# Kernel optimization log

Measured on AMD Instinct MI355X. Metric: run time of the kernel, lower is better.

## Reference

```python
import jax, jax.numpy as jnp
import numpy as np

DIM = 768        # channel dim C
HEADS = 12       # num_heads
MAXLEN = 128     # max_seq_len == window length N
NW = 64          # num_windows
B = 4            # batch


def setup_inputs() -> dict:
    key = jax.random.key(0)
    k0, k1, k2, k3 = jax.random.split(key, 4)
    B_ = NW * B
    x = jax.random.normal(k0, (B_, MAXLEN, DIM), jnp.float32)
    mask = jnp.zeros((NW, MAXLEN, MAXLEN), jnp.float32)  # 0/-inf additive window mask
    qkv_w = jax.random.normal(k1, (3 * DIM, DIM), jnp.float32) * 0.02
    bias_table = jax.random.normal(k2, (2 * MAXLEN - 1, HEADS), jnp.float32) * 0.02
    proj_w = jax.random.normal(k3, (DIM, DIM), jnp.float32) * 0.02
    proj_b = jnp.zeros((DIM,), jnp.float32)
    return {"x": x, "mask": mask, "qkv_w": qkv_w, "bias_table": bias_table,
            "proj_w": proj_w, "proj_b": proj_b}


def reference(x, mask, qkv_w, bias_table, proj_w, proj_b):
    B_, N, C = x.shape
    H = HEADS
    hd = C // H
    scale = hd ** -0.5
    # qkv projection (no bias): (B_, N, 3, H, hd)
    qkv = (x @ qkv_w.T).reshape(B_, N, 3, H, hd)
    q = qkv[:, :, 0].transpose(0, 2, 1, 3) * scale  # (B_, H, N, hd)
    k = qkv[:, :, 1].transpose(0, 2, 1, 3)
    v = qkv[:, :, 2].transpose(0, 2, 1, 3)
    attn = jnp.einsum('bhnd,bhmd->bhnm', q, k)       # (B_, H, N, N)
    # relative position bias gather
    coords = jnp.arange(N)
    rel_idx = coords[:, None] - coords[None, :] + (MAXLEN - 1)  # (N, N)
    bias = bias_table[rel_idx]                        # (N, N, H)
    attn = attn + bias.transpose(2, 0, 1)[None]       # (B_, H, N, N)
    # window mask add (mask ndim == 3 branch)
    nW = mask.shape[0]
    attn = attn.reshape(B_ // nW, nW, H, N, N) + mask[None, :, None]
    attn = jax.nn.softmax(attn.reshape(B_, H, N, N), axis=-1)
    out = jnp.einsum('bhnm,bhmd->bhnd', attn, v)      # (B_, H, N, hd)
    out = out.transpose(0, 2, 1, 3).reshape(B_, N, C)
    return out @ proj_w.T + proj_b
```

## Files before the change

### kernel.cpp

```cpp
#include <hip/hip_runtime.h>
#include <hip/hip_bf16.h>
#include <stdint.h>

typedef unsigned short u16;
typedef __bf16 bf16x8 __attribute__((ext_vector_type(8)));
typedef float f32x4 __attribute__((ext_vector_type(4)));

__device__ __forceinline__ u16 f2bf(float f) {
  union { float f; uint32_t u; } v; v.f = f;
  uint32_t u = v.u;
  return (u16)((u + 0x7FFFu + ((u >> 16) & 1u)) >> 16);
}

__device__ __forceinline__ f32x4 mfma16(bf16x8 a, bf16x8 b, f32x4 c) {
  return __builtin_amdgcn_mfma_f32_16x16x32_bf16(a, b, c, 0, 0, 0);
}

#define GLOBAL_TO_LDS16(g, l)                                                  \
  __builtin_amdgcn_global_load_lds(                                            \
      (const __attribute__((address_space(1))) void*)(g),                      \
      (__attribute__((address_space(3))) void*)(l), 16, 0, 0)

__global__ void cvt_bf16(const float* __restrict__ src, u16* __restrict__ dst, int n4) {
  int i = blockIdx.x * 256 + threadIdx.x;
  if (i < n4) {
    float4 f = ((const float4*)src)[i];
    ushort4 o;
    o.x = f2bf(f.x); o.y = f2bf(f.y); o.z = f2bf(f.z); o.w = f2bf(f.w);
    ((ushort4*)dst)[i] = o;
  }
}

__global__ __launch_bounds__(256) void qkv_gemm(
    const u16* __restrict__ A, const u16* __restrict__ Bt,
    u16* __restrict__ q, u16* __restrict__ k, u16* __restrict__ vT) {
  const int K = 768;
  __shared__ u16 As[128 * 64];
  __shared__ u16 Bs[128 * 64];
  int tid = threadIdx.x;
  int wave = tid >> 6, lane = tid & 63;
  int quad = lane >> 4, lrow = lane & 15;
  int m0 = blockIdx.y * 128, n0 = blockIdx.x * 128;
  int wr = (wave >> 1) * 64, wc = (wave & 1) * 64;

  const u16* asrc[4]; const u16* bsrc[4]; int ldst[4];
#pragma unroll
  for (int s = 0; s < 4; s++) {
    int p = (wave * 4 + s) * 64 + lane;
    int row = p >> 3, cp = p & 7;
    int c = cp ^ (row & 7);
    asrc[s] = A + (size_t)(m0 + row) * K + c * 8;
    bsrc[s] = Bt + (size_t)(n0 + row) * K + c * 8;
    ldst[s] = p * 8;
  }
  f32x4 acc[4][4] = {};
  for (int k0 = 0; k0 < K; k0 += 64) {
#pragma unroll
    for (int s = 0; s < 4; s++) {
      GLOBAL_TO_LDS16(asrc[s] + k0, As + ldst[s]);
      GLOBAL_TO_LDS16(bsrc[s] + k0, Bs + ldst[s]);
    }
    __syncthreads();
#pragma unroll
    for (int kk = 0; kk < 2; kk++) {
      bf16x8 av[4], bv[4];
#pragma unroll
      for (int i = 0; i < 4; i++) {
        int r = wr + i * 16 + lrow;
        av[i] = *(const bf16x8*)(As + r * 64 + ((((kk << 2) | quad) ^ (r & 7)) << 3));
      }
#pragma unroll
      for (int j = 0; j < 4; j++) {
        int r = wc + j * 16 + lrow;
        bv[j] = *(const bf16x8*)(Bs + r * 64 + ((((kk << 2) | quad) ^ (r & 7)) << 3));
      }
#pragma unroll
      for (int i = 0; i < 4; i++)
#pragma unroll
        for (int j = 0; j < 4; j++)
          acc[i][j] = mfma16(av[i], bv[j], acc[i][j]);
    }
    __syncthreads();
  }
#pragma unroll
  for (int j = 0; j < 4; j++) {
    int nb = n0 + wc + j * 16;
    int t = nb / 768;
    int rem = nb - t * 768;
    int h = rem >> 6;
    int d = (rem & 63) + lrow;
#pragma unroll
    for (int i = 0; i < 4; i++) {
#pragma unroll
      for (int r = 0; r < 4; r++) {
        int m = m0 + wr + i * 16 + quad * 4 + r;
        int b = m >> 7, seq = m & 127;
        size_t base = ((size_t)(b * 12 + h)) * 8192;
        float val = acc[i][j][r];
        if (t == 0)      q[base + seq * 64 + d] = f2bf(val * 0.125f);
        else if (t == 1) k[base + seq * 64 + d] = f2bf(val);
        else             vT[base + d * 128 + seq] = f2bf(val);
      }
    }
  }
}

__global__ __launch_bounds__(256) void attn_kernel(
    const u16* __restrict__ q, const u16* __restrict__ k, const u16* __restrict__ vT,
    const float* __restrict__ mask, const float* __restrict__ bias_table,
    u16* __restrict__ attn_out) {
  __shared__ u16 qk_s[2 * 128 * 72];
  __shared__ u16 vTs[64][136];
  __shared__ float bias_s[255];
  u16* qs = qk_s;
  u16* ks = qk_s + 128 * 72;
  u16* ps = qk_s;
  int tid = threadIdx.x;
  int wave = tid >> 6, lane = tid & 63;
  int quad = lane >> 4, lrow = lane & 15;
  int bh = blockIdx.x;
  int b = bh / 12, h = bh - b * 12;
  int w = b & 63;
  if (tid < 255) bias_s[tid] = bias_table[tid * 12 + h];
  int lr = tid >> 3, lc = (tid & 7) * 8;
  const u16* qg = q + (size_t)bh * 8192;
  const u16* kg = k + (size_t)bh * 8192;
  const u16* vg = vT + (size_t)bh * 8192;
#pragma unroll
  for (int r = 0; r < 4; r++) {
    *(uint4*)(qs + (lr + 32 * r) * 72 + lc) = *(const uint4*)(qg + (lr + 32 * r) * 64 + lc);
    *(uint4*)(ks + (lr + 32 * r) * 72 + lc) = *(const uint4*)(kg + (lr + 32 * r) * 64 + lc);
  }
  int vr = tid >> 4, vc = (tid & 15) * 8;
#pragma unroll
  for (int r = 0; r < 4; r++)
    *(uint4*)(&vTs[vr + 16 * r][vc]) = *(const uint4*)(vg + (vr + 16 * r) * 128 + vc);
  __syncthreads();

  f32x4 sacc[2][8] = {};
#pragma unroll
  for (int kk = 0; kk < 2; kk++) {
    bf16x8 av[2], bv[8];
#pragma unroll
    for (int i = 0; i < 2; i++)
      av[i] = *(const bf16x8*)(qs + (wave * 32 + i * 16 + lrow) * 72 + kk * 32 + quad * 8);
#pragma unroll
    for (int j = 0; j < 8; j++)
      bv[j] = *(const bf16x8*)(ks + (j * 16 + lrow) * 72 + kk * 32 + quad * 8);
#pragma unroll
    for (int i = 0; i < 2; i++)
#pragma unroll
      for (int j = 0; j < 8; j++)
        sacc[i][j] = mfma16(av[i], bv[j], sacc[i][j]);
  }
  const float* mrow = mask + (size_t)w * 16384;
#pragma unroll
  for (int i = 0; i < 2; i++)
#pragma unroll
    for (int j = 0; j < 8; j++)
#pragma unroll
      for (int r = 0; r < 4; r++) {
        int row = wave * 32 + i * 16 + quad * 4 + r;
        int col = j * 16 + lrow;
        sacc[i][j][r] += bias_s[row - col + 127] + mrow[row * 128 + col];
      }
#pragma unroll
  for (int i = 0; i < 2; i++)
#pragma unroll
    for (int r = 0; r < 4; r++) {
      float m = sacc[i][0][r];
#pragma unroll
      for (int j = 1; j < 8; j++) m = fmaxf(m, sacc[i][j][r]);
#pragma unroll
      for (int d = 1; d < 16; d <<= 1) m = fmaxf(m, __shfl_xor(m, d, 64));
      float sum = 0.f;
#pragma unroll
      for (int j = 0; j < 8; j++) {
        float e = __expf(sacc[i][j][r] - m);
        sacc[i][j][r] = e;
        sum += e;
      }
#pragma unroll
      for (int d = 1; d < 16; d <<= 1) sum += __shfl_xor(sum, d, 64);
      float inv = 1.f / sum;
#pragma unroll
      for (int j = 0; j < 8; j++) sacc[i][j][r] *= inv;
    }
  __syncthreads();
#pragma unroll
  for (int i = 0; i < 2; i++)
#pragma unroll
    for (int j = 0; j < 8; j++)
#pragma unroll
      for (int r = 0; r < 4; r++)
        ps[(wave * 32 + i * 16 + quad * 4 + r) * 136 + j * 16 + lrow] = f2bf(sacc[i][j][r]);
  __syncthreads();

  f32x4 oacc[2][4] = {};
#pragma unroll
  for (int kk = 0; kk < 4; kk++) {
    bf16x8 av[2], bv[4];
#pragma unroll
    for (int i = 0; i < 2; i++)
      av[i] = *(const bf16x8*)(ps + (wave * 32 + i * 16 + lrow) * 136 + kk * 32 + quad * 8);
#pragma unroll
    for (int j = 0; j < 4; j++)
      bv[j] = *(const bf16x8*)(&vTs[j * 16 + lrow][kk * 32 + quad * 8]);
#pragma unroll
    for (int i = 0; i < 2; i++)
#pragma unroll
      for (int j = 0; j < 4; j++)
        oacc[i][j] = mfma16(av[i], bv[j], oacc[i][j]);
  }
#pragma unroll
  for (int i = 0; i < 2; i++)
#pragma unroll
    for (int j = 0; j < 4; j++)
#pragma unroll
      for (int r = 0; r < 4; r++) {
        int seq = wave * 32 + i * 16 + quad * 4 + r;
        int d = j * 16 + lrow;
        attn_out[((size_t)(b * 128 + seq)) * 768 + h * 64 + d] = f2bf(oacc[i][j][r]);
      }
}

__global__ __launch_bounds__(256) void proj_gemm(
    const u16* __restrict__ A, const u16* __restrict__ Bt,
    const float* __restrict__ bias, float* __restrict__ out) {
  const int K = 768;
  __shared__ u16 As[128 * 64];
  __shared__ u16 Bs[128 * 64];
  int tid = threadIdx.x;
  int wave = tid >> 6, lane = tid & 63;
  int quad = lane >> 4, lrow = lane & 15;
  int m0 = blockIdx.y * 128, n0 = blockIdx.x * 128;
  int wr = (wave >> 1) * 64, wc = (wave & 1) * 64;

  const u16* asrc[4]; const u16* bsrc[4]; int ldst[4];
#pragma unroll
  for (int s = 0; s < 4; s++) {
    int p = (wave * 4 + s) * 64 + lane;
    int row = p >> 3, cp = p & 7;
    int c = cp ^ (row & 7);
    asrc[s] = A + (size_t)(m0 + row) * K + c * 8;
    bsrc[s] = Bt + (size_t)(n0 + row) * K + c * 8;
    ldst[s] = p * 8;
  }
  f32x4 acc[4][4] = {};
  for (int k0 = 0; k0 < K; k0 += 64) {
#pragma unroll
    for (int s = 0; s < 4; s++) {
      GLOBAL_TO_LDS16(asrc[s] + k0, As + ldst[s]);
      GLOBAL_TO_LDS16(bsrc[s] + k0, Bs + ldst[s]);
    }
    __syncthreads();
#pragma unroll
    for (int kk = 0; kk < 2; kk++) {
      bf16x8 av[4], bv[4];
#pragma unroll
      for (int i = 0; i < 4; i++) {
        int r = wr + i * 16 + lrow;
        av[i] = *(const bf16x8*)(As + r * 64 + ((((kk << 2) | quad) ^ (r & 7)) << 3));
      }
#pragma unroll
      for (int j = 0; j < 4; j++) {
        int r = wc + j * 16 + lrow;
        bv[j] = *(const bf16x8*)(Bs + r * 64 + ((((kk << 2) | quad) ^ (r & 7)) << 3));
      }
#pragma unroll
      for (int i = 0; i < 4; i++)
#pragma unroll
        for (int j = 0; j < 4; j++)
          acc[i][j] = mfma16(av[i], bv[j], acc[i][j]);
    }
    __syncthreads();
  }
#pragma unroll
  for (int i = 0; i < 4; i++)
#pragma unroll
    for (int j = 0; j < 4; j++)
#pragma unroll
      for (int r = 0; r < 4; r++) {
        int m = m0 + wr + i * 16 + quad * 4 + r;
        int n = n0 + wc + j * 16 + lrow;
        out[(size_t)m * 768 + n] = acc[i][j][r] + bias[n];
      }
}

extern "C" void kernel_launch(void* const* d_in, const int* in_sizes, int n_in,
                              void* d_out, int out_size, void* d_ws, size_t ws_size,
                              hipStream_t stream) {
  const float* x          = (const float*)d_in[0];
  const float* mask       = (const float*)d_in[1];
  const float* qkv_w      = (const float*)d_in[2];
  const float* bias_table = (const float*)d_in[3];
  const float* proj_w     = (const float*)d_in[4];
  const float* proj_b     = (const float*)d_in[5];
  float* out = (float*)d_out;
  char* ws = (char*)d_ws;
  u16* q_b    = (u16*)(ws);
  u16* k_b    = (u16*)(ws + 50331648);
  u16* vT_b   = (u16*)(ws + 100663296);
  u16* x_b    = (u16*)(ws + 150994944);
  u16* qw_b   = (u16*)(ws + 201326592);
  u16* pw_b   = (u16*)(ws + 204865536);
  u16* attn_b = x_b;

  cvt_bf16<<<24576, 256, 0, stream>>>(x, x_b, 6291456);
  cvt_bf16<<<1728, 256, 0, stream>>>(qkv_w, qw_b, 442368);
  cvt_bf16<<<576, 256, 0, stream>>>(proj_w, pw_b, 147456);
  qkv_gemm<<<dim3(18, 256), 256, 0, stream>>>(x_b, qw_b, q_b, k_b, vT_b);
  attn_kernel<<<3072, 256, 0, stream>>>(q_b, k_b, vT_b, mask, bias_table, attn_b);
  proj_gemm<<<dim3(6, 256), 256, 0, stream>>>(attn_b, pw_b, proj_b, out);
}
```

Measured before the change: 506.8 us.

## Vectorize GEMM/attention epilogue stores via operand swap and swizzle attention LDS

The QKV GEMM is split into two launches. The Q/K part swaps the MFMA operands so each lane holds four contiguous head-dim values and writes them as one 8-byte store, while the V part keeps the original order so the transposed V store is contiguous along the sequence. The attention kernel loads Q, K and V^T straight into LDS with global_load_lds using an XOR swizzle instead of padding, stores P swizzled, and swaps operands in PV so the output is written as vectors. The projection GEMM also swaps operands for float4 output and bias stores. The aim is to cut scattered 2-byte global stores and LDS bank conflicts, at the cost of an extra kernel launch.

```diff
diff --git a/kernel.cpp b/kernel.cpp
--- a/kernel.cpp
+++ b/kernel.cpp
@@ -31,8 +31,9 @@
   }
 }
 
+template <bool SWAP>
 __global__ __launch_bounds__(256) void qkv_gemm(
-    const u16* __restrict__ A, const u16* __restrict__ Bt,
+    const u16* __restrict__ A, const u16* __restrict__ Bt, int nbase,
     u16* __restrict__ q, u16* __restrict__ k, u16* __restrict__ vT) {
   const int K = 768;
   __shared__ u16 As[128 * 64];
@@ -40,7 +41,7 @@
   int tid = threadIdx.x;
   int wave = tid >> 6, lane = tid & 63;
   int quad = lane >> 4, lrow = lane & 15;
-  int m0 = blockIdx.y * 128, n0 = blockIdx.x * 128;
+  int m0 = blockIdx.y * 128, n0 = nbase + blockIdx.x * 128;
   int wr = (wave >> 1) * 64, wc = (wave & 1) * 64;
 
   const u16* asrc[4]; const u16* bsrc[4]; int ldst[4];
@@ -63,43 +64,56 @@
     __syncthreads();
 #pragma unroll
     for (int kk = 0; kk < 2; kk++) {
-      bf16x8 av[4], bv[4];
+      bf16x8 am[4], bn[4];
 #pragma unroll
       for (int i = 0; i < 4; i++) {
         int r = wr + i * 16 + lrow;
-        av[i] = *(const bf16x8*)(As + r * 64 + ((((kk << 2) | quad) ^ (r & 7)) << 3));
+        am[i] = *(const bf16x8*)(As + r * 64 + ((((kk << 2) | quad) ^ (r & 7)) << 3));
       }
 #pragma unroll
       for (int j = 0; j < 4; j++) {
         int r = wc + j * 16 + lrow;
-        bv[j] = *(const bf16x8*)(Bs + r * 64 + ((((kk << 2) | quad) ^ (r & 7)) << 3));
+        bn[j] = *(const bf16x8*)(Bs + r * 64 + ((((kk << 2) | quad) ^ (r & 7)) << 3));
       }
 #pragma unroll
       for (int i = 0; i < 4; i++)
 #pragma unroll
         for (int j = 0; j < 4; j++)
-          acc[i][j] = mfma16(av[i], bv[j], acc[i][j]);
+          acc[i][j] = SWAP ? mfma16(bn[i], am[j], acc[i][j])
+                           : mfma16(am[i], bn[j], acc[i][j]);
     }
     __syncthreads();
   }
-#pragma unroll
-  for (int j = 0; j < 4; j++) {
-    int nb = n0 + wc + j * 16;
-    int t = nb / 768;
-    int rem = nb - t * 768;
-    int h = rem >> 6;
-    int d = (rem & 63) + lrow;
+  int b = m0 >> 7;
+  if (SWAP) {
+    int t = n0 / 768;
+    float s = (t == 0) ? 0.125f : 1.0f;
+    u16* dst = (t == 0) ? q : k;
 #pragma unroll
     for (int i = 0; i < 4; i++) {
-#pragma unroll
-      for (int r = 0; r < 4; r++) {
-        int m = m0 + wr + i * 16 + quad * 4 + r;
-        int b = m >> 7, seq = m & 127;
-        size_t base = ((size_t)(b * 12 + h)) * 8192;
-        float val = acc[i][j][r];
-        if (t == 0)      q[base + seq * 64 + d] = f2bf(val * 0.125f);
-        else if (t == 1) k[base + seq * 64 + d] = f2bf(val);
-        else             vT[base + d * 128 + seq] = f2bf(val);
+      int nb = (n0 - t * 768) + wc + i * 16 + quad * 4;
+      int h = nb >> 6, d0 = nb & 63;
+#pragma unroll
+      for (int j = 0; j < 4; j++) {
+        int seq = wr + j * 16 + lrow;
+        ushort4 o;
+        o.x = f2bf(acc[i][j][0] * s); o.y = f2bf(acc[i][j][1] * s);
+        o.z = f2bf(acc[i][j][2] * s); o.w = f2bf(acc[i][j][3] * s);
+        *(ushort4*)(dst + ((size_t)(b * 12 + h)) * 8192 + seq * 64 + d0) = o;
+      }
+    }
+  } else {
+#pragma unroll
+    for (int j = 0; j < 4; j++) {
+      int nb = (n0 - 1536) + wc + j * 16 + lrow;
+      int h = nb >> 6, d = nb & 63;
+#pragma unroll
+      for (int i = 0; i < 4; i++) {
+        int seq0 = wr + i * 16 + quad * 4;
+        ushort4 o;
+        o.x = f2bf(acc[i][j][0]); o.y = f2bf(acc[i][j][1]);
+        o.z = f2bf(acc[i][j][2]); o.w = f2bf(acc[i][j][3]);
+        *(ushort4*)(vT + ((size_t)(b * 12 + h)) * 8192 + d * 128 + seq0) = o;
       }
     }
   }
@@ -109,12 +123,12 @@
     const u16* __restrict__ q, const u16* __restrict__ k, const u16* __restrict__ vT,
     const float* __restrict__ mask, const float* __restrict__ bias_table,
     u16* __restrict__ attn_out) {
-  __shared__ u16 qk_s[2 * 128 * 72];
-  __shared__ u16 vTs[64][136];
+  __shared__ u16 smem[2 * 128 * 64];
+  __shared__ u16 vTs[64 * 128];
   __shared__ float bias_s[255];
-  u16* qs = qk_s;
-  u16* ks = qk_s + 128 * 72;
-  u16* ps = qk_s;
+  u16* qs = smem;
+  u16* ks = smem + 128 * 64;
+  u16* ps = smem;
   int tid = threadIdx.x;
   int wave = tid >> 6, lane = tid & 63;
   int quad = lane >> 4, lrow = lane & 15;
@@ -122,19 +136,18 @@
   int b = bh / 12, h = bh - b * 12;
   int w = b & 63;
   if (tid < 255) bias_s[tid] = bias_table[tid * 12 + h];
-  int lr = tid >> 3, lc = (tid & 7) * 8;
   const u16* qg = q + (size_t)bh * 8192;
   const u16* kg = k + (size_t)bh * 8192;
   const u16* vg = vT + (size_t)bh * 8192;
 #pragma unroll
-  for (int r = 0; r < 4; r++) {
-    *(uint4*)(qs + (lr + 32 * r) * 72 + lc) = *(const uint4*)(qg + (lr + 32 * r) * 64 + lc);
-    *(uint4*)(ks + (lr + 32 * r) * 72 + lc) = *(const uint4*)(kg + (lr + 32 * r) * 64 + lc);
-  }
-  int vr = tid >> 4, vc = (tid & 15) * 8;
-#pragma unroll
-  for (int r = 0; r < 4; r++)
-    *(uint4*)(&vTs[vr + 16 * r][vc]) = *(const uint4*)(vg + (vr + 16 * r) * 128 + vc);
+  for (int s = 0; s < 4; s++) {
+    int p = wave * 256 + s * 64 + lane;
+    int row = p >> 3, c = (p & 7) ^ (row & 7);
+    GLOBAL_TO_LDS16(qg + row * 64 + c * 8, qs + p * 8);
+    GLOBAL_TO_LDS16(kg + row * 64 + c * 8, ks + p * 8);
+    int dd = p >> 4, cv = (p & 15) ^ (dd & 7);
+    GLOBAL_TO_LDS16(vg + dd * 128 + cv * 8, vTs + p * 8);
+  }
   __syncthreads();
 
   f32x4 sacc[2][8] = {};
@@ -142,11 +155,15 @@
   for (int kk = 0; kk < 2; kk++) {
     bf16x8 av[2], bv[8];
 #pragma unroll
-    for (int i = 0; i < 2; i++)
-      av[i] = *(const bf16x8*)(qs + (wave * 32 + i * 16 + lrow) * 72 + kk * 32 + quad * 8);
-#pragma unroll
-    for (int j = 0; j < 8; j++)
-      bv[j] = *(const bf16x8*)(ks + (j * 16 + lrow) * 72 + kk * 32 + quad * 8);
+    for (int i = 0; i < 2; i++) {
+      int r = wave * 32 + i * 16 + lrow;
+      av[i] = *(const bf16x8*)(qs + r * 64 + ((((kk << 2) | quad) ^ (r & 7)) << 3));
+    }
+#pragma unroll
+    for (int j = 0; j < 8; j++) {
+      int r = j * 16 + lrow;
+      bv[j] = *(const bf16x8*)(ks + r * 64 + ((((kk << 2) | quad) ^ (r & 7)) << 3));
+    }
 #pragma unroll
     for (int i = 0; i < 2; i++)
 #pragma unroll
@@ -192,36 +209,46 @@
 #pragma unroll
     for (int j = 0; j < 8; j++)
 #pragma unroll
-      for (int r = 0; r < 4; r++)
-        ps[(wave * 32 + i * 16 + quad * 4 + r) * 136 + j * 16 + lrow] = f2bf(sacc[i][j][r]);
+      for (int r = 0; r < 4; r++) {
+        int row = wave * 32 + i * 16 + quad * 4 + r;
+        int col = j * 16 + lrow;
+        int pos = (col >> 3) ^ (row & 7);
+        ps[row * 128 + pos * 8 + (col & 7)] = f2bf(sacc[i][j][r]);
+      }
   __syncthreads();
 
-  f32x4 oacc[2][4] = {};
+  f32x4 oacc[4][2] = {};
 #pragma unroll
   for (int kk = 0; kk < 4; kk++) {
-    bf16x8 av[2], bv[4];
-#pragma unroll
-    for (int i = 0; i < 2; i++)
-      av[i] = *(const bf16x8*)(ps + (wave * 32 + i * 16 + lrow) * 136 + kk * 32 + quad * 8);
-#pragma unroll
-    for (int j = 0; j < 4; j++)
-      bv[j] = *(const bf16x8*)(&vTs[j * 16 + lrow][kk * 32 + quad * 8]);
-#pragma unroll
-    for (int i = 0; i < 2; i++)
-#pragma unroll
-      for (int j = 0; j < 4; j++)
-        oacc[i][j] = mfma16(av[i], bv[j], oacc[i][j]);
-  }
-#pragma unroll
-  for (int i = 0; i < 2; i++)
-#pragma unroll
-    for (int j = 0; j < 4; j++)
-#pragma unroll
-      for (int r = 0; r < 4; r++) {
-        int seq = wave * 32 + i * 16 + quad * 4 + r;
-        int d = j * 16 + lrow;
-        attn_out[((size_t)(b * 128 + seq)) * 768 + h * 64 + d] = f2bf(oacc[i][j][r]);
-      }
+    bf16x8 vf[4], pf[2];
+#pragma unroll
+    for (int jd = 0; jd < 4; jd++) {
+      int r = jd * 16 + lrow;
+      vf[jd] = *(const bf16x8*)(vTs + r * 128 + ((((kk << 2) | quad) ^ (r & 7)) << 3));
+    }
+#pragma unroll
+    for (int i = 0; i < 2; i++) {
+      int r = wave * 32 + i * 16 + lrow;
+      pf[i] = *(const bf16x8*)(ps + r * 128 + ((((kk << 2) | quad) ^ (r & 7)) << 3));
+    }
+#pragma unroll
+    for (int jd = 0; jd < 4; jd++)
+#pragma unroll
+      for (int i = 0; i < 2; i++)
+        oacc[jd][i] = mfma16(vf[jd], pf[i], oacc[jd][i]);
+  }
+#pragma unroll
+  for (int jd = 0; jd < 4; jd++) {
+    int d0 = jd * 16 + quad * 4;
+#pragma unroll
+    for (int i = 0; i < 2; i++) {
+      int seq = wave * 32 + i * 16 + lrow;
+      ushort4 o;
+      o.x = f2bf(oacc[jd][i][0]); o.y = f2bf(oacc[jd][i][1]);
+      o.z = f2bf(oacc[jd][i][2]); o.w = f2bf(oacc[jd][i][3]);
+      *(ushort4*)(attn_out + ((size_t)(b * 128 + seq)) * 768 + h * 64 + d0) = o;
+    }
+  }
 }
 
 __global__ __launch_bounds__(256) void proj_gemm(
@@ -240,8 +267,7 @@
 #pragma unroll
   for (int s = 0; s < 4; s++) {
     int p = (wave * 4 + s) * 64 + lane;
-    int row = p >> 3, cp = p & 7;
-    int c = cp ^ (row & 7);
+    int row = p >> 3, c = (p & 7) ^ (row & 7);
     asrc[s] = A + (size_t)(m0 + row) * K + c * 8;
     bsrc[s] = Bt + (size_t)(n0 + row) * K + c * 8;
     ldst[s] = p * 8;
@@ -256,35 +282,38 @@
     __syncthreads();
 #pragma unroll
     for (int kk = 0; kk < 2; kk++) {
-      bf16x8 av[4], bv[4];
+      bf16x8 am[4], bn[4];
 #pragma unroll
       for (int i = 0; i < 4; i++) {
         int r = wr + i * 16 + lrow;
-        av[i] = *(const bf16x8*)(As + r * 64 + ((((kk << 2) | quad) ^ (r & 7)) << 3));
+        am[i] = *(const bf16x8*)(As + r * 64 + ((((kk << 2) | quad) ^ (r & 7)) << 3));
       }
 #pragma unroll
       for (int j = 0; j < 4; j++) {
         int r = wc + j * 16 + lrow;
-        bv[j] = *(const bf16x8*)(Bs + r * 64 + ((((kk << 2) | quad) ^ (r & 7)) << 3));
+        bn[j] = *(const bf16x8*)(Bs + r * 64 + ((((kk << 2) | quad) ^ (r & 7)) << 3));
       }
 #pragma unroll
       for (int i = 0; i < 4; i++)
 #pragma unroll
         for (int j = 0; j < 4; j++)
-          acc[i][j] = mfma16(av[i], bv[j], acc[i][j]);
+          acc[i][j] = mfma16(bn[i], am[j], acc[i][j]);
     }
     __syncthreads();
   }
 #pragma unroll
-  for (int i = 0; i < 4; i++)
-#pragma unroll
-    for (int j = 0; j < 4; j++)
-#pragma unroll
-      for (int r = 0; r < 4; r++) {
-        int m = m0 + wr + i * 16 + quad * 4 + r;
-        int n = n0 + wc + j * 16 + lrow;
-        out[(size_t)m * 768 + n] = acc[i][j][r] + bias[n];
-      }
+  for (int i = 0; i < 4; i++) {
+    int nb = n0 + wc + i * 16 + quad * 4;
+    float4 b4 = *(const float4*)(bias + nb);
+#pragma unroll
+    for (int j = 0; j < 4; j++) {
+      int m = m0 + wr + j * 16 + lrow;
+      float4 o;
+      o.x = acc[i][j][0] + b4.x; o.y = acc[i][j][1] + b4.y;
+      o.z = acc[i][j][2] + b4.z; o.w = acc[i][j][3] + b4.w;
+      *(float4*)(out + (size_t)m * 768 + nb) = o;
+    }
+  }
 }
 
 extern "C" void kernel_launch(void* const* d_in, const int* in_sizes, int n_in,
@@ -309,7 +338,8 @@
   cvt_bf16<<<24576, 256, 0, stream>>>(x, x_b, 6291456);
   cvt_bf16<<<1728, 256, 0, stream>>>(qkv_w, qw_b, 442368);
   cvt_bf16<<<576, 256, 0, stream>>>(proj_w, pw_b, 147456);
-  qkv_gemm<<<dim3(18, 256), 256, 0, stream>>>(x_b, qw_b, q_b, k_b, vT_b);
+  qkv_gemm<true><<<dim3(12, 256), 256, 0, stream>>>(x_b, qw_b, 0, q_b, k_b, vT_b);
+  qkv_gemm<false><<<dim3(6, 256), 256, 0, stream>>>(x_b, qw_b, 1536, q_b, k_b, vT_b);
   attn_kernel<<<3072, 256, 0, stream>>>(q_b, k_b, vT_b, mask, bias_table, attn_b);
   proj_gemm<<<dim3(6, 256), 256, 0, stream>>>(attn_b, pw_b, proj_b, out);
 }
```

Result: slower. 570.1 us (+12.5%).
